# Optimization experiments

Hardware: AMD Instinct MI355X
Metric: run time of the kernel (lower is better)

## Reference

```python
import jax, jax.numpy as jnp
import numpy as np

N_NODES = 50000
N_EDGES = 800000
D_FEAT = 96
OUT_DIM = 96


def setup_inputs() -> dict:
    key = jax.random.key(0)
    k1, k2, k3, k4 = jax.random.split(key, 4)
    x = jax.random.normal(k1, (N_NODES, D_FEAT), dtype=jnp.float32)
    W = jax.random.normal(k2, (D_FEAT, OUT_DIM), dtype=jnp.float32) / np.sqrt(D_FEAT)
    b = jnp.zeros((OUT_DIM,), dtype=jnp.float32)
    src = jax.random.randint(k3, (N_EDGES,), 0, N_NODES, dtype=jnp.int64)
    dst = jax.random.randint(k4, (N_EDGES,), 0, N_NODES, dtype=jnp.int64)
    return {"x": x, "W": W, "b": b, "src": src, "dst": dst}


def reference(x, W, b, src, dst):
    # GCNConv: symmetric degree normalization, transform-then-aggregate.
    ones = jnp.ones(src.shape[0], dtype=x.dtype)
    deg_out = jax.ops.segment_sum(ones, src, num_segments=N_NODES)  # [N]
    deg_in = jax.ops.segment_sum(ones, dst, num_segments=N_NODES)   # [N]
    inv_sqrt_out = jnp.where(deg_out > 0, jax.lax.rsqrt(deg_out), 0.0)
    inv_sqrt_in = jnp.where(deg_in > 0, jax.lax.rsqrt(deg_in), 0.0)

    h = x @ W  # [N, out_dim] - transform first (cheap GEMM)
    coef = inv_sqrt_out[src] * inv_sqrt_in[dst]         # [E]
    msg = h[src] * coef[:, None]                         # [E, out_dim] gather
    agg = jax.ops.segment_sum(msg, dst, num_segments=N_NODES)  # scatter-reduce
    return agg + b
```

## Files before the change

### kernel.cpp

```cpp
#include <hip/hip_runtime.h>

#define N_NODES 50000
#define N_EDGES 800000
#define DFEAT 96

#define RBITS  14
#define RSIZE  16384
#define NRANGE 4
#define NCHUNK 64
#define CHUNK_E (N_EDGES / NCHUNK)
#define HF_BLOCKS (NRANGE * NCHUNK)
#define NB 196

typedef short bf16x8 __attribute__((ext_vector_type(8)));
typedef float f32x4  __attribute__((ext_vector_type(4)));

__device__ __forceinline__ unsigned bpack(float a, float b) {
    unsigned ua = __float_as_uint(a);
    unsigned ub = __float_as_uint(b);
    ua = (ua + 0x7FFFu + ((ua >> 16) & 1u)) >> 16;
    ub = (ub + 0x7FFFu + ((ub >> 16) & 1u)) >> 16;
    return ua | (ub << 16);
}
__device__ __forceinline__ unsigned short b1(float a) {
    unsigned u = __float_as_uint(a);
    u = (u + 0x7FFFu + ((u >> 16) & 1u)) >> 16;
    return (unsigned short)u;
}

__global__ __launch_bounds__(512) void deg_hist_kernel(
    const int* __restrict__ src, const int* __restrict__ dst,
    unsigned* __restrict__ ptab) {
    __shared__ unsigned hh[RSIZE];
    int tid = threadIdx.x;
    int r = blockIdx.x & (NRANGE - 1);
    int c = blockIdx.x >> 2;
    for (int i = tid; i < RSIZE; i += 512) hh[i] = 0;
    __syncthreads();
    int lo = r << RBITS;
    const int4* s4 = (const int4*)(src + c * CHUNK_E);
    const int4* d4 = (const int4*)(dst + c * CHUNK_E);
    for (int i = tid; i < CHUNK_E / 4; i += 512) {
        int4 s = s4[i];
        int4 d = d4[i];
        unsigned a;
        a = (unsigned)(s.x - lo); if (a < RSIZE) atomicAdd(&hh[a], 1u);
        a = (unsigned)(s.y - lo); if (a < RSIZE) atomicAdd(&hh[a], 1u);
        a = (unsigned)(s.z - lo); if (a < RSIZE) atomicAdd(&hh[a], 1u);
        a = (unsigned)(s.w - lo); if (a < RSIZE) atomicAdd(&hh[a], 1u);
        a = (unsigned)(d.x - lo); if (a < RSIZE) atomicAdd(&hh[a], 0x10000u);
        a = (unsigned)(d.y - lo); if (a < RSIZE) atomicAdd(&hh[a], 0x10000u);
        a = (unsigned)(d.z - lo); if (a < RSIZE) atomicAdd(&hh[a], 0x10000u);
        a = (unsigned)(d.w - lo); if (a < RSIZE) atomicAdd(&hh[a], 0x10000u);
    }
    __syncthreads();
    unsigned* pt = ptab + ((size_t)blockIdx.x << RBITS);
    for (int i = tid; i < RSIZE; i += 512) pt[i] = hh[i];
}

__global__ __launch_bounds__(256) void deg_reduce_kernel(
    const unsigned* __restrict__ ptab, unsigned short* __restrict__ pfx,
    int* __restrict__ deg_out, int* __restrict__ deg_in,
    int* __restrict__ bsum) {
    __shared__ int ws[4];
    int tid = threadIdx.x;
    int n = blockIdx.x * 256 + tid;
    int so = 0, si = 0;
    if (n < N_NODES) {
        int r = n >> RBITS, bin = n & (RSIZE - 1);
        #pragma unroll 8
        for (int c = 0; c < NCHUNK; ++c) {
            size_t idx = (((size_t)(c * NRANGE + r)) << RBITS) + bin;
            unsigned v = ptab[idx];
            so += (int)(v & 0xffffu);
            pfx[idx] = (unsigned short)si;
            si += (int)(v >> 16);
        }
        deg_out[n] = so;
        deg_in[n]  = si;
    }
    int v = si;
    #pragma unroll
    for (int off = 32; off; off >>= 1) v += __shfl_down(v, off, 64);
    if ((tid & 63) == 0) ws[tid >> 6] = v;
    __syncthreads();
    if (tid == 0) bsum[blockIdx.x] = ws[0] + ws[1] + ws[2] + ws[3];
}

__global__ __launch_bounds__(256) void scan_final_kernel(
    const int* __restrict__ deg, const int* __restrict__ bsum,
    int* __restrict__ offs, int nb) {
    __shared__ int wsum[4];
    __shared__ int sbase;
    int tid = threadIdx.x, lane = tid & 63, wave = tid >> 6;
    int i = blockIdx.x * 256 + tid;
    int v = (i < N_NODES) ? deg[i] : 0;
    int x = v;
    #pragma unroll
    for (int off = 1; off < 64; off <<= 1) {
        int t = __shfl_up(x, off, 64);
        if (lane >= off) x += t;
    }
    if (lane == 63) wsum[wave] = x;
    if (wave == 0) {
        int s = 0;
        for (int j = lane; j < blockIdx.x; j += 64) s += bsum[j];
        #pragma unroll
        for (int off = 32; off; off >>= 1) s += __shfl_down(s, off, 64);
        if (lane == 0) sbase = s;
    }
    if (blockIdx.x == gridDim.x - 1 && wave == 1) {
        int s = 0;
        for (int j = lane; j < nb; j += 64) s += bsum[j];
        #pragma unroll
        for (int off = 32; off; off >>= 1) s += __shfl_down(s, off, 64);
        if (lane == 0) offs[N_NODES] = s;
    }
    __syncthreads();
    int wb = sbase;
    for (int w = 0; w < wave; ++w) wb += wsum[w];
    if (i < N_NODES) offs[i] = wb + x - v;
}

__global__ __launch_bounds__(512) void fill_kernel(
    const int* __restrict__ src, const int* __restrict__ dst,
    const int* __restrict__ offs, const unsigned short* __restrict__ pfx,
    int* __restrict__ csr_src) {
    __shared__ int cur[RSIZE];
    int tid = threadIdx.x;
    int r = blockIdx.x & (NRANGE - 1);
    int c = blockIdx.x >> 2;
    int lo = r << RBITS;
    const unsigned short* pf = pfx + ((size_t)blockIdx.x << RBITS);
    for (int i = tid; i < RSIZE; i += 512) {
        int gi = lo + i;
        int o = (gi < N_NODES) ? offs[gi] : 0;
        cur[i] = o + (int)pf[i];
    }
    __syncthreads();
    const int4* s4 = (const int4*)(src + c * CHUNK_E);
    const int4* d4 = (const int4*)(dst + c * CHUNK_E);
    for (int i = tid; i < CHUNK_E / 4; i += 512) {
        int4 s = s4[i];
        int4 d = d4[i];
        unsigned a;
        a = (unsigned)(d.x - lo); if (a < RSIZE) csr_src[atomicAdd(&cur[a], 1)] = s.x;
        a = (unsigned)(d.y - lo); if (a < RSIZE) csr_src[atomicAdd(&cur[a], 1)] = s.y;
        a = (unsigned)(d.z - lo); if (a < RSIZE) csr_src[atomicAdd(&cur[a], 1)] = s.z;
        a = (unsigned)(d.w - lo); if (a < RSIZE) csr_src[atomicAdd(&cur[a], 1)] = s.w;
    }
}

#define GEMM_ROWS 64
#define TLD 104
__global__ __launch_bounds__(256) void gemm_kernel(
    const float* __restrict__ x, const float* __restrict__ W,
    const int* __restrict__ deg_out, unsigned short* __restrict__ h, int nrows) {
    __shared__ unsigned short WT[96 * TLD];
    __shared__ unsigned short xA[GEMM_ROWS * TLD];
    int tid = threadIdx.x;
    int r0 = blockIdx.x * GEMM_ROWS;

    for (int i = tid; i < 48 * 96; i += 256) {
        int k2 = i / 96, n = i - k2 * 96;
        float w0 = W[(size_t)(2 * k2) * 96 + n];
        float w1 = W[(size_t)(2 * k2 + 1) * 96 + n];
        *(unsigned*)&WT[n * TLD + 2 * k2] = bpack(w0, w1);
    }
    for (int i = tid; i < GEMM_ROWS * 48; i += 256) {
        int m = i / 48, k2 = i - m * 48;
        int row = r0 + m; if (row >= nrows) row = nrows - 1;
        float2 v = *(const float2*)&x[(size_t)row * 96 + 2 * k2];
        *(unsigned*)&xA[m * TLD + 2 * k2] = bpack(v.x, v.y);
    }
    __syncthreads();

    int lane = tid & 63, wave = tid >> 6;
    int m16 = lane & 15;
    int g = lane >> 4;
    int rbase = wave * 16;

    bf16x8 afrag[3];
    #pragma unroll
    for (int ks = 0; ks < 3; ++ks)
        afrag[ks] = *(const bf16x8*)&xA[(rbase + m16) * TLD + ks * 32 + g * 8];

    f32x4 acc[6];
    #pragma unroll
    for (int nt = 0; nt < 6; ++nt) {
        f32x4 c = {0.f, 0.f, 0.f, 0.f};
        #pragma unroll
        for (int ks = 0; ks < 3; ++ks) {
            bf16x8 bfrag = *(const bf16x8*)&WT[(nt * 16 + m16) * TLD + ks * 32 + g * 8];
            c = __builtin_amdgcn_mfma_f32_16x16x32_bf16(afrag[ks], bfrag, c, 0, 0, 0);
        }
        acc[nt] = c;
    }

    float s[4];
    #pragma unroll
    for (int r = 0; r < 4; ++r) {
        int row = r0 + rbase + g * 4 + r;
        int d = (row < nrows) ? deg_out[row] : 1;
        s[r] = (d > 0) ? rsqrtf((float)d) : 0.f;
    }
    #pragma unroll
    for (int nt = 0; nt < 6; ++nt) {
        #pragma unroll
        for (int r = 0; r < 4; ++r) {
            int row = r0 + rbase + g * 4 + r;
            if (row < nrows)
                h[(size_t)row * 96 + nt * 16 + m16] = b1(acc[nt][r] * s[r]);
        }
    }
}

__device__ __forceinline__ void upadd(float* a, uint4 q) {
    a[0] += __uint_as_float(q.x << 16);
    a[1] += __uint_as_float(q.x & 0xffff0000u);
    a[2] += __uint_as_float(q.y << 16);
    a[3] += __uint_as_float(q.y & 0xffff0000u);
    a[4] += __uint_as_float(q.z << 16);
    a[5] += __uint_as_float(q.z & 0xffff0000u);
    a[6] += __uint_as_float(q.w << 16);
    a[7] += __uint_as_float(q.w & 0xffff0000u);
}

#define AGG_NODES 16
#define IDX_CAP 2048
__global__ __launch_bounds__(256) void agg_kernel(
    const unsigned short* __restrict__ h, const int* __restrict__ csr_src,
    const int* __restrict__ offs, const float* __restrict__ b,
    float* __restrict__ out) {
    __shared__ int sh_idx[IDX_CAP];
    __shared__ int sh_off[AGG_NODES + 1];
    int tid = threadIdx.x;
    int n0 = blockIdx.x * AGG_NODES;
    if (tid <= AGG_NODES) sh_off[tid] = offs[n0 + tid];
    __syncthreads();
    int s0 = sh_off[0];
    int len = sh_off[AGG_NODES] - s0;
    bool lds_ok = (len <= IDX_CAP);
    if (lds_ok) {
        for (int i = tid; i < len; i += 256) sh_idx[i] = csr_src[s0 + i];
    }
    __syncthreads();

    int node = tid >> 4;
    int lane16 = tid & 15;
    int j = lane16 & 3;
    int q = lane16 >> 2;
    int start = sh_off[node], end = sh_off[node + 1];
    float acc[24];
    #pragma unroll
    for (int i = 0; i < 24; ++i) acc[i] = 0.f;
    const uint4* hb = (const uint4*)h;

    int e = start + q;
    for (; e + 4 < end; e += 8) {
        int i0 = lds_ok ? sh_idx[e - s0] : csr_src[e];
        int i1 = lds_ok ? sh_idx[e + 4 - s0] : csr_src[e + 4];
        size_t b0 = (size_t)i0 * 12 + j;
        size_t b1 = (size_t)i1 * 12 + j;
        uint4 q0 = hb[b0], q1 = hb[b0 + 4], q2 = hb[b0 + 8];
        uint4 p0 = hb[b1], p1 = hb[b1 + 4], p2 = hb[b1 + 8];
        upadd(acc + 0, q0); upadd(acc + 8, q1); upadd(acc + 16, q2);
        upadd(acc + 0, p0); upadd(acc + 8, p1); upadd(acc + 16, p2);
    }
    if (e < end) {
        int i0 = lds_ok ? sh_idx[e - s0] : csr_src[e];
        size_t b0 = (size_t)i0 * 12 + j;
        uint4 q0 = hb[b0], q1 = hb[b0 + 4], q2 = hb[b0 + 8];
        upadd(acc + 0, q0); upadd(acc + 8, q1); upadd(acc + 16, q2);
    }
    #pragma unroll
    for (int i = 0; i < 24; ++i) {
        acc[i] += __shfl_xor(acc[i], 4, 64);
        acc[i] += __shfl_xor(acc[i], 8, 64);
    }
    if (q != 0) return;
    float inv = (end > start) ? rsqrtf((float)(end - start)) : 0.f;
    int n = n0 + node;
    #pragma unroll
    for (int g = 0; g < 3; ++g) {
        int slot = j + 4 * g;
        float4 bb0 = *(const float4*)(b + 8 * slot);
        float4 bb1 = *(const float4*)(b + 8 * slot + 4);
        float4 r0, r1;
        r0.x = acc[g * 8 + 0] * inv + bb0.x;
        r0.y = acc[g * 8 + 1] * inv + bb0.y;
        r0.z = acc[g * 8 + 2] * inv + bb0.z;
        r0.w = acc[g * 8 + 3] * inv + bb0.w;
        r1.x = acc[g * 8 + 4] * inv + bb1.x;
        r1.y = acc[g * 8 + 5] * inv + bb1.y;
        r1.z = acc[g * 8 + 6] * inv + bb1.z;
        r1.w = acc[g * 8 + 7] * inv + bb1.w;
        float4* o = (float4*)(out + (size_t)n * DFEAT + 8 * slot);
        o[0] = r0; o[1] = r1;
    }
}

extern "C" void kernel_launch(void* const* d_in, const int* in_sizes, int n_in,
                              void* d_out, int out_size, void* d_ws, size_t ws_size,
                              hipStream_t stream) {
    const float* x  = (const float*)d_in[0];
    const float* W  = (const float*)d_in[1];
    const float* b  = (const float*)d_in[2];
    const int*   src = (const int*)d_in[3];
    const int*   dst = (const int*)d_in[4];
    float* out = (float*)d_out;

    int* deg_out = (int*)d_ws;
    int* deg_in  = deg_out + N_NODES;
    int* offs    = deg_in + N_NODES;
    int* csr_src = offs + N_NODES + 1;
    int* bsum    = csr_src + N_EDGES;
    size_t off1 = (((size_t)(3 * N_NODES + 1 + N_EDGES + 256)) * 4 + 255) & ~(size_t)255;
    unsigned* ptab = (unsigned*)((char*)d_ws + off1);
    size_t off2 = off1 + ((size_t)HF_BLOCKS << RBITS) * 4;
    unsigned short* pfx = (unsigned short*)((char*)d_ws + off2);
    size_t off3 = (off2 + ((size_t)HF_BLOCKS << RBITS) * 2 + 255) & ~(size_t)255;
    unsigned short* h = (unsigned short*)((char*)d_ws + off3);

    deg_hist_kernel<<<HF_BLOCKS, 512, 0, stream>>>(src, dst, ptab);
    deg_reduce_kernel<<<NB, 256, 0, stream>>>(ptab, pfx, deg_out, deg_in, bsum);
    scan_final_kernel<<<NB, 256, 0, stream>>>(deg_in, bsum, offs, NB);
    fill_kernel<<<HF_BLOCKS, 512, 0, stream>>>(src, dst, offs, pfx, csr_src);
    gemm_kernel<<<(N_NODES + GEMM_ROWS - 1) / GEMM_ROWS, 256, 0, stream>>>(
        x, W, deg_out, h, N_NODES);
    agg_kernel<<<N_NODES / AGG_NODES, 256, 0, stream>>>(h, csr_src, offs, b, out);
}
```

Measured before the change: 147.1 us.

## Fuse CSR fill and GEMM into one launch; partition aggregation gathers by source range

Merges the CSR fill kernel and the bf16 MFMA GEMM into a single launch whose blocks branch on blockIdx, sharing LDS through a union. The goal is to let the two independent stages overlap and to drop one launch. The GEMM tile grows to 128 rows with 512 threads and float4 loads of x. The aggregation kernel now walks each node's edge list four times, gathering only sources in one 16K-node range per pass, to improve cache locality of h gathers, at the cost of re-reading indices and adding branch divergence.

```diff
diff --git a/kernel.cpp b/kernel.cpp
--- a/kernel.cpp
+++ b/kernel.cpp
@@ -122,56 +122,66 @@
     if (i < N_NODES) offs[i] = wb + x - v;
 }
 
-__global__ __launch_bounds__(512) void fill_kernel(
+#define GROWS 128
+#define NGB ((N_NODES + GROWS - 1) / GROWS)
+#define TLD 104
+
+union FGSm {
+    int cur[RSIZE];
+    struct {
+        unsigned short WT[96 * TLD];
+        unsigned short xA[GROWS * TLD];
+    } g;
+};
+
+__global__ __launch_bounds__(512) void fill_gemm_kernel(
     const int* __restrict__ src, const int* __restrict__ dst,
     const int* __restrict__ offs, const unsigned short* __restrict__ pfx,
-    int* __restrict__ csr_src) {
-    __shared__ int cur[RSIZE];
-    int tid = threadIdx.x;
-    int r = blockIdx.x & (NRANGE - 1);
-    int c = blockIdx.x >> 2;
-    int lo = r << RBITS;
-    const unsigned short* pf = pfx + ((size_t)blockIdx.x << RBITS);
-    for (int i = tid; i < RSIZE; i += 512) {
-        int gi = lo + i;
-        int o = (gi < N_NODES) ? offs[gi] : 0;
-        cur[i] = o + (int)pf[i];
-    }
-    __syncthreads();
-    const int4* s4 = (const int4*)(src + c * CHUNK_E);
-    const int4* d4 = (const int4*)(dst + c * CHUNK_E);
-    for (int i = tid; i < CHUNK_E / 4; i += 512) {
-        int4 s = s4[i];
-        int4 d = d4[i];
-        unsigned a;
-        a = (unsigned)(d.x - lo); if (a < RSIZE) csr_src[atomicAdd(&cur[a], 1)] = s.x;
-        a = (unsigned)(d.y - lo); if (a < RSIZE) csr_src[atomicAdd(&cur[a], 1)] = s.y;
-        a = (unsigned)(d.z - lo); if (a < RSIZE) csr_src[atomicAdd(&cur[a], 1)] = s.z;
-        a = (unsigned)(d.w - lo); if (a < RSIZE) csr_src[atomicAdd(&cur[a], 1)] = s.w;
-    }
-}
-
-#define GEMM_ROWS 64
-#define TLD 104
-__global__ __launch_bounds__(256) void gemm_kernel(
+    int* __restrict__ csr_src,
     const float* __restrict__ x, const float* __restrict__ W,
     const int* __restrict__ deg_out, unsigned short* __restrict__ h, int nrows) {
-    __shared__ unsigned short WT[96 * TLD];
-    __shared__ unsigned short xA[GEMM_ROWS * TLD];
+    __shared__ FGSm sm;
     int tid = threadIdx.x;
-    int r0 = blockIdx.x * GEMM_ROWS;
-
-    for (int i = tid; i < 48 * 96; i += 256) {
+
+    if (blockIdx.x < HF_BLOCKS) {
+        int r = blockIdx.x & (NRANGE - 1);
+        int c = blockIdx.x >> 2;
+        int lo = r << RBITS;
+        const unsigned short* pf = pfx + ((size_t)blockIdx.x << RBITS);
+        for (int i = tid; i < RSIZE; i += 512) {
+            int gi = lo + i;
+            int o = (gi < N_NODES) ? offs[gi] : 0;
+            sm.cur[i] = o + (int)pf[i];
+        }
+        __syncthreads();
+        const int4* s4 = (const int4*)(src + c * CHUNK_E);
+        const int4* d4 = (const int4*)(dst + c * CHUNK_E);
+        for (int i = tid; i < CHUNK_E / 4; i += 512) {
+            int4 s = s4[i];
+            int4 d = d4[i];
+            unsigned a;
+            a = (unsigned)(d.x - lo); if (a < RSIZE) csr_src[atomicAdd(&sm.cur[a], 1)] = s.x;
+            a = (unsigned)(d.y - lo); if (a < RSIZE) csr_src[atomicAdd(&sm.cur[a], 1)] = s.y;
+            a = (unsigned)(d.z - lo); if (a < RSIZE) csr_src[atomicAdd(&sm.cur[a], 1)] = s.z;
+            a = (unsigned)(d.w - lo); if (a < RSIZE) csr_src[atomicAdd(&sm.cur[a], 1)] = s.w;
+        }
+        return;
+    }
+
+    int r0 = (blockIdx.x - HF_BLOCKS) * GROWS;
+
+    for (int i = tid; i < 48 * 96; i += 512) {
         int k2 = i / 96, n = i - k2 * 96;
         float w0 = W[(size_t)(2 * k2) * 96 + n];
         float w1 = W[(size_t)(2 * k2 + 1) * 96 + n];
-        *(unsigned*)&WT[n * TLD + 2 * k2] = bpack(w0, w1);
-    }
-    for (int i = tid; i < GEMM_ROWS * 48; i += 256) {
-        int m = i / 48, k2 = i - m * 48;
+        *(unsigned*)&sm.g.WT[n * TLD + 2 * k2] = bpack(w0, w1);
+    }
+    for (int i = tid; i < GROWS * 24; i += 512) {
+        int m = i / 24, k4 = i - m * 24;
         int row = r0 + m; if (row >= nrows) row = nrows - 1;
-        float2 v = *(const float2*)&x[(size_t)row * 96 + 2 * k2];
-        *(unsigned*)&xA[m * TLD + 2 * k2] = bpack(v.x, v.y);
+        float4 v = *(const float4*)&x[(size_t)row * 96 + 4 * k4];
+        *(unsigned*)&sm.g.xA[m * TLD + 4 * k4]     = bpack(v.x, v.y);
+        *(unsigned*)&sm.g.xA[m * TLD + 4 * k4 + 2] = bpack(v.z, v.w);
     }
     __syncthreads();
 
@@ -183,7 +193,7 @@
     bf16x8 afrag[3];
     #pragma unroll
     for (int ks = 0; ks < 3; ++ks)
-        afrag[ks] = *(const bf16x8*)&xA[(rbase + m16) * TLD + ks * 32 + g * 8];
+        afrag[ks] = *(const bf16x8*)&sm.g.xA[(rbase + m16) * TLD + ks * 32 + g * 8];
 
     f32x4 acc[6];
     #pragma unroll
@@ -191,7 +201,7 @@
         f32x4 c = {0.f, 0.f, 0.f, 0.f};
         #pragma unroll
         for (int ks = 0; ks < 3; ++ks) {
-            bf16x8 bfrag = *(const bf16x8*)&WT[(nt * 16 + m16) * TLD + ks * 32 + g * 8];
+            bf16x8 bfrag = *(const bf16x8*)&sm.g.WT[(nt * 16 + m16) * TLD + ks * 32 + g * 8];
             c = __builtin_amdgcn_mfma_f32_16x16x32_bf16(afrag[ks], bfrag, c, 0, 0, 0);
         }
         acc[nt] = c;
@@ -228,6 +238,7 @@
 
 #define AGG_NODES 16
 #define IDX_CAP 2048
+#define NPASS 4
 __global__ __launch_bounds__(256) void agg_kernel(
     const unsigned short* __restrict__ h, const int* __restrict__ csr_src,
     const int* __restrict__ offs, const float* __restrict__ b,
@@ -256,22 +267,30 @@
     for (int i = 0; i < 24; ++i) acc[i] = 0.f;
     const uint4* hb = (const uint4*)h;
 
-    int e = start + q;
-    for (; e + 4 < end; e += 8) {
-        int i0 = lds_ok ? sh_idx[e - s0] : csr_src[e];
-        int i1 = lds_ok ? sh_idx[e + 4 - s0] : csr_src[e + 4];
-        size_t b0 = (size_t)i0 * 12 + j;
-        size_t b1 = (size_t)i1 * 12 + j;
-        uint4 q0 = hb[b0], q1 = hb[b0 + 4], q2 = hb[b0 + 8];
-        uint4 p0 = hb[b1], p1 = hb[b1 + 4], p2 = hb[b1 + 8];
-        upadd(acc + 0, q0); upadd(acc + 8, q1); upadd(acc + 16, q2);
-        upadd(acc + 0, p0); upadd(acc + 8, p1); upadd(acc + 16, p2);
-    }
-    if (e < end) {
-        int i0 = lds_ok ? sh_idx[e - s0] : csr_src[e];
-        size_t b0 = (size_t)i0 * 12 + j;
-        uint4 q0 = hb[b0], q1 = hb[b0 + 4], q2 = hb[b0 + 8];
-        upadd(acc + 0, q0); upadd(acc + 8, q1); upadd(acc + 16, q2);
+    for (int pass = 0; pass < NPASS; ++pass) {
+        int e = start + q;
+        for (; e + 4 < end; e += 8) {
+            int i0 = lds_ok ? sh_idx[e - s0] : csr_src[e];
+            int i1 = lds_ok ? sh_idx[e + 4 - s0] : csr_src[e + 4];
+            if ((i0 >> RBITS) == pass) {
+                size_t b0 = (size_t)i0 * 12 + j;
+                uint4 q0 = hb[b0], q1 = hb[b0 + 4], q2 = hb[b0 + 8];
+                upadd(acc + 0, q0); upadd(acc + 8, q1); upadd(acc + 16, q2);
+            }
+            if ((i1 >> RBITS) == pass) {
+                size_t b1 = (size_t)i1 * 12 + j;
+                uint4 p0 = hb[b1], p1 = hb[b1 + 4], p2 = hb[b1 + 8];
+                upadd(acc + 0, p0); upadd(acc + 8, p1); upadd(acc + 16, p2);
+            }
+        }
+        if (e < end) {
+            int i0 = lds_ok ? sh_idx[e - s0] : csr_src[e];
+            if ((i0 >> RBITS) == pass) {
+                size_t b0 = (size_t)i0 * 12 + j;
+                uint4 q0 = hb[b0], q1 = hb[b0 + 4], q2 = hb[b0 + 8];
+                upadd(acc + 0, q0); upadd(acc + 8, q1); upadd(acc + 16, q2);
+            }
+        }
     }
     #pragma unroll
     for (int i = 0; i < 24; ++i) {
@@ -325,8 +344,7 @@
     deg_hist_kernel<<<HF_BLOCKS, 512, 0, stream>>>(src, dst, ptab);
     deg_reduce_kernel<<<NB, 256, 0, stream>>>(ptab, pfx, deg_out, deg_in, bsum);
     scan_final_kernel<<<NB, 256, 0, stream>>>(deg_in, bsum, offs, NB);
-    fill_kernel<<<HF_BLOCKS, 512, 0, stream>>>(src, dst, offs, pfx, csr_src);
-    gemm_kernel<<<(N_NODES + GEMM_ROWS - 1) / GEMM_ROWS, 256, 0, stream>>>(
-        x, W, deg_out, h, N_NODES);
+    fill_gemm_kernel<<<HF_BLOCKS + NGB, 512, 0, stream>>>(
+        src, dst, offs, pfx, csr_src, x, W, deg_out, h, N_NODES);
     agg_kernel<<<N_NODES / AGG_NODES, 256, 0, stream>>>(h, csr_src, offs, b, out);
 }
```

Result: no change. 149.1 us (+1.3%).

## Split aggregation feature dimension into three slices across separate blocks

Applied to the files above, without the earlier changes.

The aggregation kernel now launches three times as many blocks. Each block handles one 32-feature slice of the 96 output columns for its 16 nodes, so each thread keeps 8 accumulators instead of 24. The edge loop is unrolled to four independent gathers per iteration. The aim is more parallelism, lower register pressure and more loads in flight. The cost is that each block reloads the CSR indices and offsets three times, and each gathered row is split into 16-byte pieces fetched by different blocks, which may hurt cache locality.

```diff
diff --git a/kernel.cpp b/kernel.cpp
--- a/kernel.cpp
+++ b/kernel.cpp
@@ -228,6 +228,8 @@
 
 #define AGG_NODES 16
 #define IDX_CAP 2048
+#define NSLICE 3
+#define NBLK_N (N_NODES / AGG_NODES)
 __global__ __launch_bounds__(256) void agg_kernel(
     const unsigned short* __restrict__ h, const int* __restrict__ csr_src,
     const int* __restrict__ offs, const float* __restrict__ b,
@@ -235,7 +237,8 @@
     __shared__ int sh_idx[IDX_CAP];
     __shared__ int sh_off[AGG_NODES + 1];
     int tid = threadIdx.x;
-    int n0 = blockIdx.x * AGG_NODES;
+    int slice = blockIdx.x / NBLK_N;
+    int n0 = (blockIdx.x - slice * NBLK_N) * AGG_NODES;
     if (tid <= AGG_NODES) sh_off[tid] = offs[n0 + tid];
     __syncthreads();
     int s0 = sh_off[0];
@@ -251,53 +254,51 @@
     int j = lane16 & 3;
     int q = lane16 >> 2;
     int start = sh_off[node], end = sh_off[node + 1];
-    float acc[24];
-    #pragma unroll
-    for (int i = 0; i < 24; ++i) acc[i] = 0.f;
+    float acc[8];
+    #pragma unroll
+    for (int i = 0; i < 8; ++i) acc[i] = 0.f;
     const uint4* hb = (const uint4*)h;
+    int sj = slice * 4 + j;
 
     int e = start + q;
-    for (; e + 4 < end; e += 8) {
+    for (; e + 12 < end; e += 16) {
+        int i0 = lds_ok ? sh_idx[e - s0]      : csr_src[e];
+        int i1 = lds_ok ? sh_idx[e + 4 - s0]  : csr_src[e + 4];
+        int i2 = lds_ok ? sh_idx[e + 8 - s0]  : csr_src[e + 8];
+        int i3 = lds_ok ? sh_idx[e + 12 - s0] : csr_src[e + 12];
+        uint4 q0 = hb[(size_t)i0 * 12 + sj];
+        uint4 q1 = hb[(size_t)i1 * 12 + sj];
+        uint4 q2 = hb[(size_t)i2 * 12 + sj];
+        uint4 q3 = hb[(size_t)i3 * 12 + sj];
+        upadd(acc, q0); upadd(acc, q1); upadd(acc, q2); upadd(acc, q3);
+    }
+    for (; e < end; e += 4) {
         int i0 = lds_ok ? sh_idx[e - s0] : csr_src[e];
-        int i1 = lds_ok ? sh_idx[e + 4 - s0] : csr_src[e + 4];
-        size_t b0 = (size_t)i0 * 12 + j;
-        size_t b1 = (size_t)i1 * 12 + j;
-        uint4 q0 = hb[b0], q1 = hb[b0 + 4], q2 = hb[b0 + 8];
-        uint4 p0 = hb[b1], p1 = hb[b1 + 4], p2 = hb[b1 + 8];
-        upadd(acc + 0, q0); upadd(acc + 8, q1); upadd(acc + 16, q2);
-        upadd(acc + 0, p0); upadd(acc + 8, p1); upadd(acc + 16, p2);
-    }
-    if (e < end) {
-        int i0 = lds_ok ? sh_idx[e - s0] : csr_src[e];
-        size_t b0 = (size_t)i0 * 12 + j;
-        uint4 q0 = hb[b0], q1 = hb[b0 + 4], q2 = hb[b0 + 8];
-        upadd(acc + 0, q0); upadd(acc + 8, q1); upadd(acc + 16, q2);
-    }
-    #pragma unroll
-    for (int i = 0; i < 24; ++i) {
+        uint4 q0 = hb[(size_t)i0 * 12 + sj];
+        upadd(acc, q0);
+    }
+    #pragma unroll
+    for (int i = 0; i < 8; ++i) {
         acc[i] += __shfl_xor(acc[i], 4, 64);
         acc[i] += __shfl_xor(acc[i], 8, 64);
     }
     if (q != 0) return;
     float inv = (end > start) ? rsqrtf((float)(end - start)) : 0.f;
     int n = n0 + node;
-    #pragma unroll
-    for (int g = 0; g < 3; ++g) {
-        int slot = j + 4 * g;
-        float4 bb0 = *(const float4*)(b + 8 * slot);
-        float4 bb1 = *(const float4*)(b + 8 * slot + 4);
-        float4 r0, r1;
-        r0.x = acc[g * 8 + 0] * inv + bb0.x;
-        r0.y = acc[g * 8 + 1] * inv + bb0.y;
-        r0.z = acc[g * 8 + 2] * inv + bb0.z;
-        r0.w = acc[g * 8 + 3] * inv + bb0.w;
-        r1.x = acc[g * 8 + 4] * inv + bb1.x;
-        r1.y = acc[g * 8 + 5] * inv + bb1.y;
-        r1.z = acc[g * 8 + 6] * inv + bb1.z;
-        r1.w = acc[g * 8 + 7] * inv + bb1.w;
-        float4* o = (float4*)(out + (size_t)n * DFEAT + 8 * slot);
-        o[0] = r0; o[1] = r1;
-    }
+    int c0 = slice * 32 + j * 8;
+    float4 bb0 = *(const float4*)(b + c0);
+    float4 bb1 = *(const float4*)(b + c0 + 4);
+    float4 r0, r1;
+    r0.x = acc[0] * inv + bb0.x;
+    r0.y = acc[1] * inv + bb0.y;
+    r0.z = acc[2] * inv + bb0.z;
+    r0.w = acc[3] * inv + bb0.w;
+    r1.x = acc[4] * inv + bb1.x;
+    r1.y = acc[5] * inv + bb1.y;
+    r1.z = acc[6] * inv + bb1.z;
+    r1.w = acc[7] * inv + bb1.w;
+    float4* o = (float4*)(out + (size_t)n * DFEAT + c0);
+    o[0] = r0; o[1] = r1;
 }
 
 extern "C" void kernel_launch(void* const* d_in, const int* in_sizes, int n_in,
@@ -328,5 +329,5 @@
     fill_kernel<<<HF_BLOCKS, 512, 0, stream>>>(src, dst, offs, pfx, csr_src);
     gemm_kernel<<<(N_NODES + GEMM_ROWS - 1) / GEMM_ROWS, 256, 0, stream>>>(
         x, W, deg_out, h, N_NODES);
-    agg_kernel<<<N_NODES / AGG_NODES, 256, 0, stream>>>(h, csr_src, offs, b, out);
-}
+    agg_kernel<<<NSLICE * NBLK_N, 256, 0, stream>>>(h, csr_src, offs, b, out);
+}
```

New measurement: 155.8 us. 1.06x slower.
